# Optimization experiments

Measured on AMD Instinct MI355X. Metric: run time of the kernel, lower is better.

The kernel has to match this reference:

```python
import jax, jax.numpy as jnp
import numpy as np

NEG = -1e9


def _lstm_step(x, h, c, W_ih, W_hh, b_ih, b_hh):
    # torch LSTM gate order: i, f, g, o
    gates = x @ W_ih.T + b_ih + h @ W_hh.T + b_hh
    i, f, g, o = jnp.split(gates, 4, axis=-1)
    c_new = jax.nn.sigmoid(f) * c + jax.nn.sigmoid(i) * jnp.tanh(g)
    h_new = jax.nn.sigmoid(o) * jnp.tanh(c_new)
    return h_new, c_new


def _forward(encoder_states, emb, W_ih, W_hh, b_ih, b_hh, W_att,
             pad_mask, pointer_mask, token_ids, target_sequence,
             sos_token, eos_token, output_len):
    B, N, D = encoder_states.shape
    V = emb.shape[0]
    dt = encoder_states.dtype
    padf = pad_mask.astype(dt)
    enc = encoder_states * padf[..., None]          # zero padded node states
    # _init_lstm_state: mean of encoder states over valid nodes (pad-only mask)
    h0 = enc.sum(axis=1) / padf.sum(axis=1, keepdims=True)  # [B, D]
    # attention mask after pointer restriction: only valid leaf pointer nodes
    attn_mask = jnp.where(pointer_mask, jnp.asarray(0.0, dt), jnp.asarray(NEG, dt))
    n_ptr = pointer_mask.sum(axis=1).astype(dt)     # [B]
    thr = 1.0 / n_ptr                               # _threshold_cf = 1.0
    b_idx = jnp.arange(B)

    # teacher forcing: step 1 uses SOS, step s>1 uses target_sequence[s-1]
    sos_row = jnp.full((1, B), sos_token, dtype=target_sequence.dtype)
    inputs = jnp.concatenate([sos_row, target_sequence[1:output_len - 1]], axis=0)  # [T-1, B]

    def step(carry, inp):
        h, c = carry
        x = emb[inp]                                     # [B, E]
        h, c = _lstm_step(x, h, c, W_ih, W_hh, b_ih, b_hh)
        # Luong attention -> probabilities over tree nodes
        scores = jnp.einsum('bnd,bd->bn', enc, h @ W_att.T) + attn_mask
        probs = jax.nn.softmax(scores, axis=1)           # [B, N]
        # threshold: probabilities below 1/n_ptr are zeroed; only pointer nodes kept
        probs = jnp.where(pointer_mask & (probs >= thr[:, None]), probs, jnp.asarray(0.0, dt))
        # scatter(reduce='sum') node probabilities into vocab-sized output
        out = jnp.zeros((B, V), dt).at[b_idx[:, None], token_ids].add(probs)
        out = out.at[:, eos_token].set(1.0 - probs.sum(axis=1))
        return (h, c), out

    (_, _), outs = jax.lax.scan(step, (h0, h0), inputs)   # [T-1, B, V]
    out0 = jnp.zeros((B, V), dt).at[:, sos_token].set(1.0)
    return jnp.concatenate([out0[None], outs], axis=0)    # [T, B, V]


def setup_inputs() -> dict:
    key = jax.random.key(0)
    ks = jax.random.split(key, 10)
    B, N, D, E, V, T = 32, 2048, 512, 512, 32000, 32
    encoder_states = jax.random.normal(ks[0], (B, N, D), dtype=jnp.float32)
    lengths = jax.random.randint(ks[1], (B,), N // 2, N + 1)
    pad_mask = jnp.arange(N)[None, :] < lengths[:, None]            # [B, N] ragged trees
    leaf = jax.random.bernoulli(ks[2], 0.5, (B, N))
    pointer_mask = pad_mask & leaf                                  # valid leaf pointer nodes
    token_ids = jax.random.randint(ks[3], (B, N), 0, V, dtype=jnp.int32)
    target_sequence = jax.random.randint(ks[4], (T, B), 3, V, dtype=jnp.int32)
    s = 0.02
    emb = jax.random.normal(ks[5], (V, E), dtype=jnp.float32) * s
    W_ih = jax.random.normal(ks[6], (4 * D, E), dtype=jnp.float32) * s
    W_hh = jax.random.normal(ks[7], (4 * D, D), dtype=jnp.float32) * s
    b_ih = jnp.zeros((4 * D,), dtype=jnp.float32)
    b_hh = jnp.zeros((4 * D,), dtype=jnp.float32)
    W_att = jax.random.normal(ks[8], (D, D), dtype=jnp.float32) * s
    return {
        'encoder_states': encoder_states, 'emb': emb,
        'W_ih': W_ih, 'W_hh': W_hh, 'b_ih': b_ih, 'b_hh': b_hh, 'W_att': W_att,
        'pad_mask': pad_mask, 'pointer_mask': pointer_mask,
        'token_ids': token_ids, 'target_sequence': target_sequence,
        'sos_token': 1, 'eos_token': 2, 'output_len': T,
    }


def reference(encoder_states, emb, W_ih, W_hh, b_ih, b_hh, W_att,
              pad_mask, pointer_mask, token_ids, target_sequence,
              sos_token, eos_token, output_len):
    return _forward(encoder_states, emb, W_ih, W_hh, b_ih, b_hh, W_att,
                    pad_mask, pointer_mask, token_ids, target_sequence,
                    sos_token, eos_token, output_len)
```

## Files before the change

kernel.cpp:

```cpp
#include <hip/hip_runtime.h>
#include <math.h>

#define BB 32
#define NN 2048
#define DD 512
#define VV 32000
#define NSTEP 31

__device__ inline float sigm(float x){ return 1.0f/(1.0f+expf(-x)); }
__device__ inline float dot4(float4 a, float4 b){
  return a.x*b.x + a.y*b.y + a.z*b.z + a.w*b.w;
}

__device__ inline float red8(float a0,float a1,float a2,float a3,
                             float a4,float a5,float a6,float a7,int lane){
  float m01 = ((lane&1)? a1:a0) + __shfl_xor(((lane&1)? a0:a1),1,64);
  float m23 = ((lane&1)? a3:a2) + __shfl_xor(((lane&1)? a2:a3),1,64);
  float m45 = ((lane&1)? a5:a4) + __shfl_xor(((lane&1)? a4:a5),1,64);
  float m67 = ((lane&1)? a7:a6) + __shfl_xor(((lane&1)? a6:a7),1,64);
  float m03 = ((lane&2)? m23:m01) + __shfl_xor(((lane&2)? m01:m23),2,64);
  float m47 = ((lane&2)? m67:m45) + __shfl_xor(((lane&2)? m45:m67),2,64);
  float m   = ((lane&4)? m47:m03) + __shfl_xor(((lane&4)? m03:m47),4,64);
  m += __shfl_xor(m,8,64); m += __shfl_xor(m,16,64); m += __shfl_xor(m,32,64);
  return m;
}

__device__ inline uint4 fresh_load4(const unsigned int* p){
  uint4 r;
  asm volatile("global_load_dwordx4 %0, %1, off sc0 sc1\n\t"
               "s_waitcnt vmcnt(0)"
               : "=&v"(r) : "v"(p) : "memory");
  return r;
}

__global__ __launch_bounds__(256) void k_cnt(
    const int* __restrict__ pad, const int* __restrict__ pmask,
    const int* __restrict__ sosp,
    float* __restrict__ cntp, float* __restrict__ thr, float* __restrict__ out,
    unsigned int* __restrict__ flags) {
  __shared__ int r1[256], r2[256];
  int b = blockIdx.x, tid = threadIdx.x;
  if (b == 0 && tid < 256)
    __hip_atomic_store(&flags[tid], 0u, __ATOMIC_RELAXED,
                       __HIP_MEMORY_SCOPE_AGENT);
  float4* orow4 = (float4*)(out + (size_t)b*VV);
  float4 z = {0.f,0.f,0.f,0.f};
  for (int i = tid; i < VV/4; i += 256) orow4[i] = z;
  int cp = 0, cq = 0;
  for (int n = tid; n < NN; n += 256) { cp += pad[b*NN+n]; cq += pmask[b*NN+n]; }
  r1[tid] = cp; r2[tid] = cq; __syncthreads();
  for (int st = 128; st; st >>= 1) {
    if (tid < st) { r1[tid] += r1[tid+st]; r2[tid] += r2[tid+st]; }
    __syncthreads();
  }
  if (tid == 0) {
    cntp[b] = (float)r1[0];
    thr[b]  = 1.0f/(float)r2[0];
    out[(size_t)b*VV + sosp[0]] = 1.0f;
  }
}

__global__ __launch_bounds__(128) void k_meanpart(
    const float* __restrict__ enc, const int* __restrict__ pad,
    float* __restrict__ hpart) {
  int b = blockIdx.x, ch = blockIdx.y, kq = threadIdx.x;
  int n0 = ch*32;
  float4 acc = {0.f,0.f,0.f,0.f};
#pragma unroll 8
  for (int r = 0; r < 32; r++) {
    int n = n0 + r;
    float msk = (float)pad[b*NN + n];
    float4 v = *(const float4*)(enc + ((size_t)(b*NN + n))*DD + kq*4);
    acc.x += msk*v.x; acc.y += msk*v.y; acc.z += msk*v.z; acc.w += msk*v.w;
  }
  *(float4*)(hpart + ((size_t)(b*64 + ch))*DD + kq*4) = acc;
}

__global__ __launch_bounds__(128) void k_meanfin(
    const float* __restrict__ hpart, const float* __restrict__ cntp,
    float* __restrict__ h0, float* __restrict__ c) {
  int b = blockIdx.x, kq = threadIdx.x;
  float4 acc = {0.f,0.f,0.f,0.f};
  for (int ch = 0; ch < 64; ch++) {
    float4 v = *(const float4*)(hpart + ((size_t)(b*64 + ch))*DD + kq*4);
    acc.x += v.x; acc.y += v.y; acc.z += v.z; acc.w += v.w;
  }
  float ic = 1.0f/cntp[b];
  acc.x *= ic; acc.y *= ic; acc.z *= ic; acc.w *= ic;
  *(float4*)(h0 + b*DD + kq*4) = acc;
  *(float4*)(c  + b*DD + kq*4) = acc;
}

__global__ __launch_bounds__(512, 2) void k_hloop(
    const float* __restrict__ h0, const float* __restrict__ Whh,
    const float* __restrict__ Wih, const float* __restrict__ bih,
    const float* __restrict__ bhh, const float* __restrict__ emb,
    const float* __restrict__ Watt, const int* __restrict__ target,
    const int* __restrict__ sosp, float* __restrict__ H,
    float* __restrict__ Q, unsigned int* __restrict__ flags) {
  __shared__ float spad[20736];
  float* g   = spad;
  float* Gls = spad + 256;
  int bi = blockIdx.x, d0 = bi*2;
  int tid = threadIdx.x;
  int w = tid>>6, lane = tid&63;
  float4 W0[8], W1[8], Wi0[8], Wi1[8], Wa0[2], Wa1[2];
#pragma unroll
  for (int j = 0; j < 8; j++) {
    int r = (j>>1)*DD + d0 + (j&1);
    const float* wp = Whh + (size_t)r*DD + lane*4;
    W0[j]  = *(const float4*)wp; W1[j]  = *(const float4*)(wp + 256);
    const float* ip = Wih + (size_t)r*DD + lane*4;
    Wi0[j] = *(const float4*)ip; Wi1[j] = *(const float4*)(ip + 256);
  }
#pragma unroll
  for (int e = 0; e < 2; e++) {
    const float* ap = Watt + (size_t)(d0+e)*DD + lane*4;
    Wa0[e] = *(const float4*)ap; Wa1[e] = *(const float4*)(ap + 256);
  }
  int jrole = lane & 7;
  int brow = (jrole>>1)*DD + d0 + (jrole&1);
  float biasj = bih[brow] + bhh[brow];
  int pb = tid>>1, pdd = tid&1;
  float creg = 0.f;
  if (tid < 64) creg = h0[pb*DD + d0 + pdd];

  {
    int sos = sosp[0];
    const float* xp = emb + (size_t)sos*DD + lane*4;
    float4 x0 = *(const float4*)xp, x1 = *(const float4*)(xp + 256);
    float a0 = dot4(x0,Wi0[0]) + dot4(x1,Wi1[0]);
    float a1 = dot4(x0,Wi0[1]) + dot4(x1,Wi1[1]);
    float a2 = dot4(x0,Wi0[2]) + dot4(x1,Wi1[2]);
    float a3 = dot4(x0,Wi0[3]) + dot4(x1,Wi1[3]);
    float a4 = dot4(x0,Wi0[4]) + dot4(x1,Wi1[4]);
    float a5 = dot4(x0,Wi0[5]) + dot4(x1,Wi1[5]);
    float a6 = dot4(x0,Wi0[6]) + dot4(x1,Wi1[6]);
    float a7 = dot4(x0,Wi0[7]) + dot4(x1,Wi1[7]);
    float v = red8(a0,a1,a2,a3,a4,a5,a6,a7,lane);
    if (lane < 8) {
      float vb = v + biasj;
#pragma unroll
      for (int bb = 0; bb < 4; bb++) Gls[(w*4+bb)*8 + lane] = vb;
    }
  }
  __syncthreads();

  float4 h0s[4], h1s[4];
  for (int s = 0; s < NSTEP; s++) {
#pragma unroll
    for (int j = 0; j < 8; j++) {
      asm volatile("" : "+v"(W0[j].x), "+v"(W0[j].y),
                        "+v"(W0[j].z), "+v"(W0[j].w),
                        "+v"(W1[j].x), "+v"(W1[j].y),
                        "+v"(W1[j].z), "+v"(W1[j].w));
      asm volatile("" : "+v"(Wi0[j].x), "+v"(Wi0[j].y),
                        "+v"(Wi0[j].z), "+v"(Wi0[j].w),
                        "+v"(Wi1[j].x), "+v"(Wi1[j].y),
                        "+v"(Wi1[j].z), "+v"(Wi1[j].w));
    }
#pragma unroll
    for (int e = 0; e < 2; e++) {
      asm volatile("" : "+v"(Wa0[e].x), "+v"(Wa0[e].y),
                        "+v"(Wa0[e].z), "+v"(Wa0[e].w),
                        "+v"(Wa1[e].x), "+v"(Wa1[e].y),
                        "+v"(Wa1[e].z), "+v"(Wa1[e].w));
    }
    const float* hin = (s == 0) ? h0 : (H + (size_t)(s-1)*BB*DD);
#pragma unroll
    for (int bb = 0; bb < 4; bb++) {
      int b = w*4 + bb;
      const float* hp = hin + b*DD + lane*4;
      float4 h0v = *(const float4*)hp, h1v = *(const float4*)(hp + 256);
      h0s[bb] = h0v; h1s[bb] = h1v;
      float a0 = dot4(h0v,W0[0]) + dot4(h1v,W1[0]);
      float a1 = dot4(h0v,W0[1]) + dot4(h1v,W1[1]);
      float a2 = dot4(h0v,W0[2]) + dot4(h1v,W1[2]);
      float a3 = dot4(h0v,W0[3]) + dot4(h1v,W1[3]);
      float a4 = dot4(h0v,W0[4]) + dot4(h1v,W1[4]);
      float a5 = dot4(h0v,W0[5]) + dot4(h1v,W1[5]);
      float a6 = dot4(h0v,W0[6]) + dot4(h1v,W1[6]);
      float a7 = dot4(h0v,W0[7]) + dot4(h1v,W1[7]);
      float v = red8(a0,a1,a2,a3,a4,a5,a6,a7,lane);
      if (lane < 8) g[b*8 + lane] = v;
    }
    float4 xg0[4], xg1[4];
    if (s < NSTEP-1) {
#pragma unroll
      for (int bb = 0; bb < 4; bb++) {
        int tg = target[(s+1)*BB + w*4 + bb];
        const float* xp = emb + (size_t)tg*DD + lane*4;
        xg0[bb] = *(const float4*)xp; xg1[bb] = *(const float4*)(xp + 256);
      }
    }
    __syncthreads();
    if (tid < 64) {
      const float* Gs = Gls + (s&1)*256;
      float gi = g[pb*8 + 0 + pdd] + Gs[pb*8 + 0 + pdd];
      float gf = g[pb*8 + 2 + pdd] + Gs[pb*8 + 2 + pdd];
      float gg = g[pb*8 + 4 + pdd] + Gs[pb*8 + 4 + pdd];
      float go = g[pb*8 + 6 + pdd] + Gs[pb*8 + 6 + pdd];
      creg = sigm(gf)*creg + sigm(gi)*tanhf(gg);
      float hn = sigm(go)*tanhf(creg);
      __hip_atomic_store(H + (size_t)s*BB*DD + pb*DD + d0 + pdd, hn,
                         __ATOMIC_RELAXED, __HIP_MEMORY_SCOPE_AGENT);
    }
    __syncthreads();
    unsigned tgt = (unsigned)(s+1);
    if (tid == 0)
      __hip_atomic_store(&flags[bi], tgt,
                         __ATOMIC_RELAXED, __HIP_MEMORY_SCOPE_AGENT);
    if (s < NSTEP-1) {
      float* Gd = Gls + ((s+1)&1)*256;
#pragma unroll
      for (int bb = 0; bb < 4; bb++) {
        float a0 = dot4(xg0[bb],Wi0[0]) + dot4(xg1[bb],Wi1[0]);
        float a1 = dot4(xg0[bb],Wi0[1]) + dot4(xg1[bb],Wi1[1]);
        float a2 = dot4(xg0[bb],Wi0[2]) + dot4(xg1[bb],Wi1[2]);
        float a3 = dot4(xg0[bb],Wi0[3]) + dot4(xg1[bb],Wi1[3]);
        float a4 = dot4(xg0[bb],Wi0[4]) + dot4(xg1[bb],Wi1[4]);
        float a5 = dot4(xg0[bb],Wi0[5]) + dot4(xg1[bb],Wi1[5]);
        float a6 = dot4(xg0[bb],Wi0[6]) + dot4(xg1[bb],Wi1[6]);
        float a7 = dot4(xg0[bb],Wi0[7]) + dot4(xg1[bb],Wi1[7]);
        float v = red8(a0,a1,a2,a3,a4,a5,a6,a7,lane);
        if (lane < 8) Gd[(w*4+bb)*8 + lane] = v + biasj;
      }
    }
    if (s > 0) {
#pragma unroll
      for (int bb = 0; bb < 4; bb++) {
        float q0 = dot4(h0s[bb],Wa0[0]) + dot4(h1s[bb],Wa1[0]);
        float q1 = dot4(h0s[bb],Wa0[1]) + dot4(h1s[bb],Wa1[1]);
        float v = red8(q0,q1,0.f,0.f,0.f,0.f,0.f,0.f,lane);
        if (lane < 2)
          Q[((size_t)(s-1)*BB + w*4 + bb)*DD + d0 + lane] = v;
      }
    }
    if (tid < 64) {
      const unsigned int* fp = flags + tid*4;
      for (;;) {
        uint4 f = fresh_load4(fp);
        bool ok = f.x >= tgt && f.y >= tgt && f.z >= tgt && f.w >= tgt;
        if (__all(ok)) break;
        __builtin_amdgcn_s_sleep(1);
      }
    }
    __syncthreads();
  }

#pragma unroll
  for (int bb = 0; bb < 4; bb++) {
    int b = w*4 + bb;
    const float* hp = H + (size_t)(NSTEP-1)*BB*DD + b*DD + lane*4;
    float4 h0v = *(const float4*)hp, h1v = *(const float4*)(hp + 256);
    float q0 = dot4(h0v,Wa0[0]) + dot4(h1v,Wa1[0]);
    float q1 = dot4(h0v,Wa0[1]) + dot4(h1v,Wa1[1]);
    float v = red8(q0,q1,0.f,0.f,0.f,0.f,0.f,0.f,lane);
    if (lane < 2)
      Q[((size_t)(NSTEP-1)*BB + b)*DD + d0 + lane] = v;
  }
}

__global__ __launch_bounds__(256) void k_scores3(
    const float* __restrict__ enc, const float* __restrict__ Q,
    float* __restrict__ S) {
  int nt = blockIdx.x, b = blockIdx.y;
  int w = threadIdx.x>>6, lane = threadIdx.x&63;
  int s0 = w*8;
  float4 q0[8], q1[8];
#pragma unroll
  for (int j = 0; j < 8; j++) {
    const float* qp = Q + (size_t)((s0 + j)*BB + b)*DD + lane*4;
    q0[j] = *(const float4*)qp; q1[j] = *(const float4*)(qp + 256);
  }
  int n0 = nt*32;
  int sl = s0 + (lane & 7);
#pragma unroll 2
  for (int i = 0; i < 32; i++) {
    int n = n0 + i;
    const float* ep = enc + ((size_t)(b*NN + n))*DD + lane*4;
    float4 e0 = *(const float4*)ep, e1 = *(const float4*)(ep + 256);
    float a0 = dot4(e0,q0[0]) + dot4(e1,q1[0]);
    float a1 = dot4(e0,q0[1]) + dot4(e1,q1[1]);
    float a2 = dot4(e0,q0[2]) + dot4(e1,q1[2]);
    float a3 = dot4(e0,q0[3]) + dot4(e1,q1[3]);
    float a4 = dot4(e0,q0[4]) + dot4(e1,q1[4]);
    float a5 = dot4(e0,q0[5]) + dot4(e1,q1[5]);
    float a6 = dot4(e0,q0[6]) + dot4(e1,q1[6]);
    float a7 = dot4(e0,q0[7]) + dot4(e1,q1[7]);
    float v = red8(a0,a1,a2,a3,a4,a5,a6,a7,lane);
    if (lane < 8 && sl < NSTEP) S[((size_t)sl*BB + b)*NN + n] = v;
  }
}

__global__ __launch_bounds__(256) void k_scatter2(
    const float* __restrict__ S, const int* __restrict__ pmask,
    const int* __restrict__ tok, const float* __restrict__ thr,
    const int* __restrict__ eosp, float* __restrict__ out) {
  __shared__ float red[256];
  __shared__ float ex[NN];
  int s = blockIdx.x, b = blockIdx.y, tid = threadIdx.x;
  float* orow = out + ((size_t)(s+1)*BB + b)*VV;
  float4 z = {0.f,0.f,0.f,0.f};
  float4* orow4 = (float4*)orow;
  for (int i = tid; i < VV/4; i += 256) orow4[i] = z;
  const float* sr = S + ((size_t)s*BB + b)*NN;
  const int* pm = pmask + b*NN;
  float m = -3.4e38f;
  for (int n = tid; n < NN; n += 256) if (pm[n]) m = fmaxf(m, sr[n]);
  red[tid] = m; __syncthreads();
  for (int st = 128; st; st >>= 1) {
    if (tid < st) red[tid] = fmaxf(red[tid], red[tid+st]);
    __syncthreads();
  }
  float smax = red[0]; __syncthreads();
  float sum = 0.f;
  for (int n = tid; n < NN; n += 256) {
    float e = pm[n] ? expf(sr[n] - smax) : 0.f;
    ex[n] = e; sum += e;
  }
  red[tid] = sum; __syncthreads();
  for (int st = 128; st; st >>= 1) {
    if (tid < st) red[tid] += red[tid+st];
    __syncthreads();
  }
  float inv = 1.0f/red[0];
  float th = thr[b];
  float keep = 0.f;
  for (int n = tid; n < NN; n += 256) {
    float p = ex[n]*inv;
    if (p >= th) { atomicAdd(orow + tok[b*NN + n], p); keep += p; }
  }
  __syncthreads();
  red[tid] = keep; __syncthreads();
  for (int st = 128; st; st >>= 1) {
    if (tid < st) red[tid] += red[tid+st];
    __syncthreads();
  }
  if (tid == 0) orow[eosp[0]] = 1.0f - red[0];
}

extern "C" void kernel_launch(void* const* d_in, const int* in_sizes, int n_in,
                              void* d_out, int out_size, void* d_ws, size_t ws_size,
                              hipStream_t stream) {
  const float* enc   = (const float*)d_in[0];
  const float* emb   = (const float*)d_in[1];
  const float* Wih   = (const float*)d_in[2];
  const float* Whh   = (const float*)d_in[3];
  const float* bih   = (const float*)d_in[4];
  const float* bhh   = (const float*)d_in[5];
  const float* Watt  = (const float*)d_in[6];
  const int*   pad   = (const int*)d_in[7];
  const int*   pmask = (const int*)d_in[8];
  const int*   tok   = (const int*)d_in[9];
  const int*   target= (const int*)d_in[10];
  const int*   sosp  = (const int*)d_in[11];
  const int*   eosp  = (const int*)d_in[12];
  float* out = (float*)d_out;

  float* w    = (float*)d_ws;
  float* c    = w;
  float* h0   = c    + BB*DD;
  float* H    = h0   + BB*DD;
  float* Q    = H    + NSTEP*BB*DD;
  float* S    = Q    + 32*BB*DD;
  float* G0   = S    + (size_t)NSTEP*BB*NN;
  float* cntp = G0   + (size_t)992*2048;
  float* thr  = cntp + 32;
  unsigned int* flags = (unsigned int*)(thr + 32);
  float* hpart = G0;

  k_cnt<<<32, 256, 0, stream>>>(pad, pmask, sosp, cntp, thr, out, flags);
  k_meanpart<<<dim3(32,64), 128, 0, stream>>>(enc, pad, hpart);
  k_meanfin<<<32, 128, 0, stream>>>(hpart, cntp, h0, c);

  k_hloop<<<256, 512, 0, stream>>>(h0, Whh, Wih, bih, bhh, emb, Watt, target,
                                   sosp, H, Q, flags);

  k_scores3<<<dim3(64,32), 256, 0, stream>>>(enc, Q, S);
  k_scatter2<<<dim3(NSTEP,32), 256, 0, stream>>>(S, pmask, tok, thr, eosp, out);
}
```

Before: 598.7 us.

## Use a master-block barrier and per-wave gate slices to drop a block sync

Two sync changes in the persistent recurrence kernel. First, each wave now does its own LSTM cell update on the gate slice it computed, which removes one __syncthreads per step. Second, the grid barrier changes: only block 0 polls all 256 per-block flags and then publishes a release flag, and every other block spins on that one word. Fewer agents polling many flags should cut memory traffic, but the barrier now needs an extra hop through the master block on each step.

```diff
diff --git a/kernel.cpp b/kernel.cpp
--- a/kernel.cpp
+++ b/kernel.cpp
@@ -40,9 +40,14 @@
     unsigned int* __restrict__ flags) {
   __shared__ int r1[256], r2[256];
   int b = blockIdx.x, tid = threadIdx.x;
-  if (b == 0 && tid < 256)
-    __hip_atomic_store(&flags[tid], 0u, __ATOMIC_RELAXED,
-                       __HIP_MEMORY_SCOPE_AGENT);
+  if (b == 0) {
+    if (tid < 256)
+      __hip_atomic_store(&flags[tid], 0u, __ATOMIC_RELAXED,
+                         __HIP_MEMORY_SCOPE_AGENT);
+    if (tid == 0)
+      __hip_atomic_store(&flags[256], 0u, __ATOMIC_RELAXED,
+                         __HIP_MEMORY_SCOPE_AGENT);
+  }
   float4* orow4 = (float4*)(out + (size_t)b*VV);
   float4 z = {0.f,0.f,0.f,0.f};
   for (int i = tid; i < VV/4; i += 256) orow4[i] = z;
@@ -99,11 +104,11 @@
     const int* __restrict__ sosp, float* __restrict__ H,
     float* __restrict__ Q, unsigned int* __restrict__ flags) {
   __shared__ float spad[20736];
-  float* g   = spad;
-  float* Gls = spad + 256;
   int bi = blockIdx.x, d0 = bi*2;
   int tid = threadIdx.x;
   int w = tid>>6, lane = tid&63;
+  float* gw = spad + w*32;
+  float* Gb = spad + 256;
   float4 W0[8], W1[8], Wi0[8], Wi1[8], Wa0[2], Wa1[2];
 #pragma unroll
   for (int j = 0; j < 8; j++) {
@@ -121,9 +126,10 @@
   int jrole = lane & 7;
   int brow = (jrole>>1)*DD + d0 + (jrole&1);
   float biasj = bih[brow] + bhh[brow];
-  int pb = tid>>1, pdd = tid&1;
+  int bloc = lane>>1, pdd = lane&1;
+  int bmy = w*4 + bloc;
   float creg = 0.f;
-  if (tid < 64) creg = h0[pb*DD + d0 + pdd];
+  if (lane < 8) creg = h0[bmy*DD + d0 + pdd];
 
   {
     int sos = sosp[0];
@@ -140,8 +146,9 @@
     float v = red8(a0,a1,a2,a3,a4,a5,a6,a7,lane);
     if (lane < 8) {
       float vb = v + biasj;
-#pragma unroll
-      for (int bb = 0; bb < 4; bb++) Gls[(w*4+bb)*8 + lane] = vb;
+      float* Gd = Gb + w*32;
+#pragma unroll
+      for (int bb = 0; bb < 4; bb++) Gd[bb*8 + lane] = vb;
     }
   }
   __syncthreads();
@@ -182,7 +189,7 @@
       float a6 = dot4(h0v,W0[6]) + dot4(h1v,W1[6]);
       float a7 = dot4(h0v,W0[7]) + dot4(h1v,W1[7]);
       float v = red8(a0,a1,a2,a3,a4,a5,a6,a7,lane);
-      if (lane < 8) g[b*8 + lane] = v;
+      if (lane < 8) gw[bb*8 + lane] = v;
     }
     float4 xg0[4], xg1[4];
     if (s < NSTEP-1) {
@@ -193,16 +200,15 @@
         xg0[bb] = *(const float4*)xp; xg1[bb] = *(const float4*)(xp + 256);
       }
     }
-    __syncthreads();
-    if (tid < 64) {
-      const float* Gs = Gls + (s&1)*256;
-      float gi = g[pb*8 + 0 + pdd] + Gs[pb*8 + 0 + pdd];
-      float gf = g[pb*8 + 2 + pdd] + Gs[pb*8 + 2 + pdd];
-      float gg = g[pb*8 + 4 + pdd] + Gs[pb*8 + 4 + pdd];
-      float go = g[pb*8 + 6 + pdd] + Gs[pb*8 + 6 + pdd];
+    if (lane < 8) {
+      const float* Gs = Gb + (s&1)*256 + w*32;
+      float gi = gw[bloc*8 + 0 + pdd] + Gs[bloc*8 + 0 + pdd];
+      float gf = gw[bloc*8 + 2 + pdd] + Gs[bloc*8 + 2 + pdd];
+      float gg = gw[bloc*8 + 4 + pdd] + Gs[bloc*8 + 4 + pdd];
+      float go = gw[bloc*8 + 6 + pdd] + Gs[bloc*8 + 6 + pdd];
       creg = sigm(gf)*creg + sigm(gi)*tanhf(gg);
       float hn = sigm(go)*tanhf(creg);
-      __hip_atomic_store(H + (size_t)s*BB*DD + pb*DD + d0 + pdd, hn,
+      __hip_atomic_store(H + (size_t)s*BB*DD + bmy*DD + d0 + pdd, hn,
                          __ATOMIC_RELAXED, __HIP_MEMORY_SCOPE_AGENT);
     }
     __syncthreads();
@@ -211,7 +217,7 @@
       __hip_atomic_store(&flags[bi], tgt,
                          __ATOMIC_RELAXED, __HIP_MEMORY_SCOPE_AGENT);
     if (s < NSTEP-1) {
-      float* Gd = Gls + ((s+1)&1)*256;
+      float* Gd = Gb + ((s+1)&1)*256 + w*32;
 #pragma unroll
       for (int bb = 0; bb < 4; bb++) {
         float a0 = dot4(xg0[bb],Wi0[0]) + dot4(xg1[bb],Wi1[0]);
@@ -223,7 +229,7 @@
         float a6 = dot4(xg0[bb],Wi0[6]) + dot4(xg1[bb],Wi1[6]);
         float a7 = dot4(xg0[bb],Wi0[7]) + dot4(xg1[bb],Wi1[7]);
         float v = red8(a0,a1,a2,a3,a4,a5,a6,a7,lane);
-        if (lane < 8) Gd[(w*4+bb)*8 + lane] = v + biasj;
+        if (lane < 8) Gd[bb*8 + lane] = v + biasj;
       }
     }
     if (s > 0) {
@@ -236,14 +242,23 @@
           Q[((size_t)(s-1)*BB + w*4 + bb)*DD + d0 + lane] = v;
       }
     }
-    if (tid < 64) {
-      const unsigned int* fp = flags + tid*4;
-      for (;;) {
-        uint4 f = fresh_load4(fp);
-        bool ok = f.x >= tgt && f.y >= tgt && f.z >= tgt && f.w >= tgt;
-        if (__all(ok)) break;
+    if (bi == 0) {
+      if (tid < 64) {
+        const unsigned int* fp = flags + tid*4;
+        for (;;) {
+          uint4 f = fresh_load4(fp);
+          bool ok = f.x >= tgt && f.y >= tgt && f.z >= tgt && f.w >= tgt;
+          if (__all(ok)) break;
+          __builtin_amdgcn_s_sleep(1);
+        }
+        if (tid == 0)
+          __hip_atomic_store(&flags[256], tgt,
+                             __ATOMIC_RELAXED, __HIP_MEMORY_SCOPE_AGENT);
+      }
+    } else if (tid == 0) {
+      while (__hip_atomic_load(&flags[256], __ATOMIC_RELAXED,
+                               __HIP_MEMORY_SCOPE_AGENT) < tgt)
         __builtin_amdgcn_s_sleep(1);
-      }
     }
     __syncthreads();
   }
```

After: 616.9 us. 3.0% more time.
